# Kernel optimization log

Hardware: AMD Instinct MI355X
Metric: run time of the kernel (lower is better)

## Reference

```python
import jax, jax.numpy as jnp
import numpy as np

B = 256        # graphs per batch (python loop in original, vectorized here)
N = 512        # nodes per graph
DEG = 16       # avg degree
E_PER = N * DEG
T = 64         # num_node_types
D = 128        # gnn_hidden_dim


def setup_inputs() -> dict:
    key = jax.random.key(0)
    ks = jax.random.split(key, 8)
    node_feat = jax.random.randint(ks[0], (B * N,), 0, T)
    offs = (jnp.arange(B) * N)[:, None]
    src = (jax.random.randint(ks[1], (B, E_PER), 0, N) + offs).reshape(-1)
    dst = (jax.random.randint(ks[2], (B, E_PER), 0, N) + offs).reshape(-1)
    emb_table = jax.random.normal(ks[3], (T, D), dtype=jnp.float32) * 0.02
    W1 = jax.random.normal(ks[4], (D, D), dtype=jnp.float32) * (1.0 / np.sqrt(D))
    b1 = jnp.zeros((D,), dtype=jnp.float32)
    W2 = jax.random.normal(ks[5], (D, D), dtype=jnp.float32) * (1.0 / np.sqrt(D))
    b2 = jnp.zeros((D,), dtype=jnp.float32)
    return {"node_feat": node_feat, "src": src, "dst": dst,
            "emb_table": emb_table, "W1": W1, "b1": b1, "W2": W2, "b2": b2}


def _gcn_layer(h, src, dst, out_isqrt, in_isqrt, W, b, n):
    # DGL GraphConv, norm='both': D_in^{-1/2} A D_out^{-1/2} h W + b
    m = (h * out_isqrt[:, None])[src]                      # [E, D] gather
    agg = jax.ops.segment_sum(m, dst, num_segments=n)      # [Ntot, D] scatter
    return (agg * in_isqrt[:, None]) @ W + b


def reference(node_feat, src, dst, emb_table, W1, b1, W2, b2):
    n = node_feat.shape[0]
    ones = jnp.ones(src.shape[0], dtype=emb_table.dtype)
    deg_out = jnp.clip(jax.ops.segment_sum(ones, src, num_segments=n), 1.0)
    deg_in = jnp.clip(jax.ops.segment_sum(ones, dst, num_segments=n), 1.0)
    out_isqrt = jax.lax.rsqrt(deg_out)
    in_isqrt = jax.lax.rsqrt(deg_in)

    h = emb_table[node_feat]                                # [Ntot, D]
    # layer 1 (dropout is eval-mode identity) + relu, layer 2 + relu
    h = jax.nn.relu(_gcn_layer(h, src, dst, out_isqrt, in_isqrt, W1, b1, n))
    h = jax.nn.relu(_gcn_layer(h, src, dst, out_isqrt, in_isqrt, W2, b2, n))

    # dgl.mean_nodes per graph, then mean_gnn_embeddings + stack -> [B, D]
    gid = jnp.arange(n) // N
    hg = jax.ops.segment_sum(h, gid, num_segments=B) / float(N)
    return hg
```

## Files before the change

### kernel.cpp

```cpp
#include <hip/hip_runtime.h>
#include <stdint.h>

#define GRAPHS 256
#define NPG    512
#define EPG    8192
#define NTOT   (GRAPHS*NPG)

typedef __attribute__((ext_vector_type(8))) short s16x8;
typedef __attribute__((ext_vector_type(4))) float f32x4;

__device__ __forceinline__ float bf2f(unsigned short u){
  union { unsigned int i; float f; } c; c.i = ((unsigned int)u)<<16; return c.f;
}
__device__ __forceinline__ unsigned short f2bf(float f){
  union { float f; unsigned int i; } c; c.f = f;
  unsigned int r = c.i + 0x7fffu + ((c.i>>16)&1u);
  return (unsigned short)(r>>16);
}

__global__ __launch_bounds__(512) void k_csr(const int* __restrict__ src,
      const int* __restrict__ dst, const int* __restrict__ ntype,
      const float* __restrict__ emb, const float* __restrict__ W1,
      const float* __restrict__ W2,
      unsigned short* __restrict__ sorted_g, int* __restrict__ start_g,
      float* __restrict__ out_isqrt, unsigned short* __restrict__ EW1T,
      unsigned short* __restrict__ W2T){
  __shared__ int hist[NPG], cursor[NPG], co[NPG], cs[NPG+1];
  __shared__ unsigned short ntype_sh[NPG];
  __shared__ unsigned short sorted[EPG];
  const int tid=threadIdx.x;
  if (blockIdx.x >= GRAPHS){
    const int gid = (blockIdx.x-GRAPHS)*512 + tid;
    if (gid < 8192){
      const int t = gid>>7, c = gid&127;
      float acc=0.f;
      #pragma unroll 4
      for (int k=0;k<128;k++) acc += emb[t*128+k]*W1[k*128+c];
      EW1T[c*64+t]=f2bf(acc);
    } else {
      const int i = gid - 8192;
      const int k = i>>7, n = i&127;
      W2T[n*128+k] = f2bf(W2[k*128+n]);
    }
    return;
  }
  const int b=blockIdx.x, eb=b*EPG, nb=b*NPG;
  hist[tid]=0; co[tid]=0; ntype_sh[tid]=(unsigned short)ntype[nb+tid];
  __syncthreads();
  int4 d4[4], s4[4];
  {
    const int4* dv = (const int4*)(dst+eb);
    const int4* sv = (const int4*)(src+eb);
    #pragma unroll
    for (int j=0;j<4;j++){
      d4[j]=dv[tid + j*512];
      s4[j]=sv[tid + j*512];
      atomicAdd(&hist[d4[j].x&(NPG-1)],1); atomicAdd(&hist[d4[j].y&(NPG-1)],1);
      atomicAdd(&hist[d4[j].z&(NPG-1)],1); atomicAdd(&hist[d4[j].w&(NPG-1)],1);
      atomicAdd(&co[s4[j].x&(NPG-1)],1);   atomicAdd(&co[s4[j].y&(NPG-1)],1);
      atomicAdd(&co[s4[j].z&(NPG-1)],1);   atomicAdd(&co[s4[j].w&(NPG-1)],1);
    }
  }
  __syncthreads();
  if (tid<64){
    int carry=0;
    #pragma unroll
    for (int c=0;c<8;c++){
      int sc=hist[64*c+tid];
      #pragma unroll
      for (int off=1;off<64;off<<=1){ int y=__shfl_up(sc,off); if (tid>=off) sc+=y; }
      cs[64*c+tid+1]=carry+sc;
      carry+=__shfl(sc,63);
    }
    if (tid==0) cs[0]=0;
  }
  __syncthreads();
  cursor[tid]=cs[tid];
  __syncthreads();
  #pragma unroll
  for (int j=0;j<4;j++){
    int dl, s, pos;
    dl=d4[j].x&(NPG-1); s=s4[j].x&(NPG-1);
    pos=atomicAdd(&cursor[dl],1); sorted[pos]=(unsigned short)((ntype_sh[s]<<9)|s);
    dl=d4[j].y&(NPG-1); s=s4[j].y&(NPG-1);
    pos=atomicAdd(&cursor[dl],1); sorted[pos]=(unsigned short)((ntype_sh[s]<<9)|s);
    dl=d4[j].z&(NPG-1); s=s4[j].z&(NPG-1);
    pos=atomicAdd(&cursor[dl],1); sorted[pos]=(unsigned short)((ntype_sh[s]<<9)|s);
    dl=d4[j].w&(NPG-1); s=s4[j].w&(NPG-1);
    pos=atomicAdd(&cursor[dl],1); sorted[pos]=(unsigned short)((ntype_sh[s]<<9)|s);
  }
  __syncthreads();
  for (int i=tid;i<EPG/2;i+=512)
    ((unsigned int*)(sorted_g+(size_t)eb))[i] = ((const unsigned int*)sorted)[i];
  if (tid==0) start_g[b*(NPG+1)+NPG]=cs[NPG];
  start_g[b*(NPG+1)+tid]=cs[tid];
  {
    int a=co[tid]; if(a<1)a=1;
    out_isqrt[nb+tid]=rsqrtf((float)a);
  }
}

#define A1_LDS 73232
__global__ __launch_bounds__(512) void k_agg1(
      const unsigned short* __restrict__ sorted_g, const int* __restrict__ start_g,
      const unsigned short* __restrict__ EW1T, const float* __restrict__ out_isqrt,
      const float* __restrict__ b1, unsigned short* __restrict__ h1F){
  extern __shared__ char smem[];
  float* S      = (float*)(smem);
  float* wsc    = (float*)(smem + 69632);
  int*   sstart = (int*)  (smem + 71680);
  float* bsh    = (float*)(smem + 72720);
  const int bid=blockIdx.x, b=bid>>1, half=bid&1;
  const int v0=half*256, nb=b*NPG, tid=threadIdx.x;
  for (int i=tid; i<(256*68)/4; i+=512) ((f32x4*)S)[i]=(f32x4){0.f,0.f,0.f,0.f};
  for (int i=tid; i<NPG; i+=512) wsc[i]=out_isqrt[nb+i];
  for (int i=tid; i<257; i+=512) sstart[i]=start_g[b*(NPG+1)+v0+i];
  if (tid<128) bsh[tid]=b1[tid];
  __syncthreads();
  if (tid<256){
    const int beg=sstart[tid], end=sstart[tid+1];
    float* Sd = S + tid*68;
    const unsigned short* sg = sorted_g + (size_t)b*EPG;
    for (int i=beg;i<end;++i){
      const int ent = sg[i];
      Sd[ent>>9] += wsc[ent&511];
    }
  }
  __syncthreads();
  const int wave=tid>>6, lane=tid&63, l16=lane&15, quad=lane>>4;
  f32x4 acc[2][8];
  #pragma unroll
  for (int rt=0;rt<2;rt++)
    #pragma unroll
    for (int nt=0;nt<8;nt++) acc[rt][nt]=(f32x4){0.f,0.f,0.f,0.f};
  #pragma unroll
  for (int ks=0; ks<4; ++ks){
    const int kc = (ks&1)*32 + quad*8;
    s16x8 a[2];
    #pragma unroll
    for (int rt=0;rt<2;rt++){
      const int m = (wave*2+rt)*16 + l16;
      const float* sp = &S[m*68 + kc];
      f32x4 va = *(const f32x4*)sp;
      f32x4 vb = *(const f32x4*)(sp+4);
      union { s16x8 v; unsigned short u[8]; } pk;
      #pragma unroll
      for (int j=0;j<8;j++){
        const float f = (j<4)? va[j] : vb[j-4];
        const unsigned short hi = f2bf(f);
        pk.u[j] = (ks<2) ? hi : f2bf(f - bf2f(hi));
      }
      a[rt]=pk.v;
    }
    #pragma unroll
    for (int nt=0;nt<8;nt++){
      s16x8 bfr=__builtin_bit_cast(s16x8,
          *(const uint4*)(EW1T + (size_t)(nt*16+l16)*64 + kc));
      #pragma unroll
      for (int rt=0;rt<2;rt++)
        acc[rt][nt]=__builtin_amdgcn_mfma_f32_16x16x32_bf16(a[rt],bfr,acc[rt][nt],0,0,0);
    }
  }
  #pragma unroll
  for (int rt=0;rt<2;rt++){
    const int W = wave*2+rt;
    const int mloc = W*16 + quad*4;
    float isq[4], os[4];
    #pragma unroll
    for (int r=0;r<4;r++){
      int d = sstart[mloc+r+1]-sstart[mloc+r]; if (d<1) d=1;
      isq[r]=rsqrtf((float)d);
      os[r]=wsc[v0+mloc+r];
    }
    const int ks2 = half*8 + (W>>1);
    const int q2  = ((W&1)<<1) | (quad>>1);
    const int j0  = (quad&1)*4;
    #pragma unroll
    for (int nt=0;nt<8;nt++){
      const int col = nt*16+l16;
      const float bb = bsh[col];
      ushort4 st;
      float v;
      v = fmaxf(acc[rt][nt][0]*isq[0]+bb,0.f)*os[0]; st.x=f2bf(v);
      v = fmaxf(acc[rt][nt][1]*isq[1]+bb,0.f)*os[1]; st.y=f2bf(v);
      v = fmaxf(acc[rt][nt][2]*isq[2]+bb,0.f)*os[2]; st.z=f2bf(v);
      v = fmaxf(acc[rt][nt][3]*isq[3]+bb,0.f)*os[3]; st.w=f2bf(v);
      const size_t off = ((((size_t)b*16 + ks2)*8 + nt)*64 + q2*16 + l16)*8 + j0;
      *(ushort4*)(h1F + off) = st;
    }
  }
}

#define A2_LDS 67080
__global__ __launch_bounds__(512) void k_agg2(
      const unsigned short* __restrict__ sorted_g, const int* __restrict__ start_g,
      const unsigned short* __restrict__ h1F, unsigned short* __restrict__ M1F){
  extern __shared__ char smem[];
  unsigned char* A = (unsigned char*)smem;
  unsigned int* A32 = (unsigned int*)smem;
  int* sstart = (int*)(smem + 66560);
  const int bid=blockIdx.x;
  const int b  = ((bid>>5)<<3) | (bid&7);
  const int dt = (bid>>3)&3;
  const int v0=dt*128, tid=threadIdx.x;
  for (int i=tid; i<66560/16; i+=512) ((uint4*)smem)[i]=(uint4){0u,0u,0u,0u};
  for (int i=tid; i<129; i+=512) sstart[i]=start_g[b*(NPG+1)+v0+i];
  __syncthreads();
  {
    const int d = tid>>2, q = tid&3;
    const int beg=sstart[d], end=sstart[d+1], len=end-beg;
    const int qb = beg + ((len*q)>>2), qe = beg + ((len*(q+1))>>2);
    const unsigned short* sg = sorted_g + (size_t)b*EPG;
    const int rowbase = d*130;
    for (int i=qb;i<qe;++i){
      const int s = sg[i]&511;
      atomicAdd(&A32[rowbase + (s>>2)], 1u<<((s&3)*8));
    }
  }
  __syncthreads();
  const int wave=tid>>6, lane=tid&63, l16=lane&15, quad=lane>>4;
  const int mg=wave>>1, ng=wave&1;
  f32x4 acc[2][4];
  #pragma unroll
  for (int rt=0;rt<2;rt++)
    #pragma unroll
    for (int ct=0;ct<4;ct++) acc[rt][ct]=(f32x4){0.f,0.f,0.f,0.f};
  const uint4* bp[4];
  #pragma unroll
  for (int ct=0;ct<4;ct++)
    bp[ct] = (const uint4*)h1F + (((size_t)b*16)*8 + (ng*4+ct))*64 + lane;
  const unsigned char* Ab[2];
  #pragma unroll
  for (int rt=0;rt<2;rt++)
    Ab[rt] = A + ((mg*2+rt)*16 + l16)*520 + quad*8;
  #pragma unroll 2
  for (int ks=0; ks<16; ++ks){
    uint4 bq[4];
    #pragma unroll
    for (int ct=0;ct<4;ct++) bq[ct] = bp[ct][(size_t)ks*512];
    s16x8 afr[2];
    #pragma unroll
    for (int rt=0;rt<2;rt++){
      const uint2 aw = *(const uint2*)(Ab[rt] + ks*32);
      union { s16x8 v; unsigned short u[8]; } pk;
      #pragma unroll
      for (int j=0;j<4;j++){
        const float f0 = (float)((aw.x>>(8*j))&0xffu);
        const float f1 = (float)((aw.y>>(8*j))&0xffu);
        pk.u[j]   = (unsigned short)(__builtin_bit_cast(unsigned int, f0)>>16);
        pk.u[j+4] = (unsigned short)(__builtin_bit_cast(unsigned int, f1)>>16);
      }
      afr[rt]=pk.v;
    }
    #pragma unroll
    for (int rt=0;rt<2;rt++)
      #pragma unroll
      for (int ct=0;ct<4;ct++)
        acc[rt][ct]=__builtin_amdgcn_mfma_f32_16x16x32_bf16(afr[rt],
            __builtin_bit_cast(s16x8, bq[ct]), acc[rt][ct],0,0,0);
  }
  #pragma unroll
  for (int rt=0;rt<2;rt++){
    const int mloc=(mg*2+rt)*16 + quad*4;
    const int M = dt*8 + mg*2 + rt;
    float isq[4];
    #pragma unroll
    for (int r=0;r<4;r++){
      int d=sstart[mloc+r+1]-sstart[mloc+r]; if (d<1) d=1;
      isq[r]=rsqrtf((float)d);
    }
    #pragma unroll
    for (int ct=0;ct<4;ct++){
      const int ks2   = ng*2 + (ct>>1);
      const int quad2 = ((ct&1)<<1) | (l16>>3);
      const int j     = l16&7;
      unsigned short* base = M1F
          + ((((size_t)b*32+M)*4+ks2)*64 + quad2*16)*8 + j;
      #pragma unroll
      for (int r=0;r<4;r++)
        base[(size_t)(quad*4+r)*8] = f2bf(acc[rt][ct][r]*isq[r]);
    }
  }
}

__global__ __launch_bounds__(512) void k_gemm2(const unsigned short* __restrict__ M1F,
      const unsigned short* __restrict__ W2T, const float* __restrict__ b2,
      float* __restrict__ out){
  __shared__ __align__(16) unsigned short WT[128][136];
  __shared__ float bsh[128];
  __shared__ float colpart[8][128];
  const int b=blockIdx.x, tid=threadIdx.x;
  for (int idx=tid; idx<2048; idx+=512){
    const int row = idx>>4, c8 = idx&15;
    *(uint4*)&WT[row][c8*8] = *(const uint4*)(W2T + row*128 + c8*8);
  }
  if (tid<128) bsh[tid]=b2[tid];
  __syncthreads();
  const int wave=tid>>6, lane=tid&63, l16=lane&15, quad=lane>>4;
  float p[8];
  #pragma unroll
  for (int i=0;i<8;i++) p[i]=0.f;
  for (int chunk=0; chunk<2; ++chunk){
    f32x4 acc[2][8];
    #pragma unroll
    for (int rt=0;rt<2;rt++)
      #pragma unroll
      for (int ct=0;ct<8;ct++) acc[rt][ct]=(f32x4){0.f,0.f,0.f,0.f};
    #pragma unroll
    for (int ks=0;ks<4;ks++){
      s16x8 a[2], bf[8];
      #pragma unroll
      for (int rt=0;rt<2;rt++){
        const int M = wave*4 + chunk*2 + rt;
        a[rt]=__builtin_bit_cast(s16x8, *(const uint4*)(M1F
            + ((((size_t)b*32+M)*4+ks)*64 + lane)*8));
      }
      #pragma unroll
      for (int ct=0;ct<8;ct++)
        bf[ct]=__builtin_bit_cast(s16x8, *(const uint4*)&WT[ct*16+l16][ks*32+quad*8]);
      #pragma unroll
      for (int rt=0;rt<2;rt++)
        #pragma unroll
        for (int ct=0;ct<8;ct++)
          acc[rt][ct]=__builtin_amdgcn_mfma_f32_16x16x32_bf16(a[rt],bf[ct],acc[rt][ct],0,0,0);
    }
    #pragma unroll
    for (int rt=0;rt<2;rt++)
      #pragma unroll
      for (int ct=0;ct<8;ct++)
        #pragma unroll
        for (int r=0;r<4;r++){
          const int col=ct*16+l16;
          p[ct] += fmaxf(acc[rt][ct][r]+bsh[col],0.f);
        }
  }
  #pragma unroll
  for (int ct=0;ct<8;ct++){
    p[ct] += __shfl_xor(p[ct],16);
    p[ct] += __shfl_xor(p[ct],32);
  }
  if (quad==0){
    #pragma unroll
    for (int ct=0;ct<8;ct++) colpart[wave][ct*16+l16]=p[ct];
  }
  __syncthreads();
  if (tid<128){
    float s=0.f;
    #pragma unroll
    for (int w=0;w<8;w++) s+=colpart[w][tid];
    out[b*128+tid]=s*(1.f/512.f);
  }
}

extern "C" void kernel_launch(void* const* d_in, const int* in_sizes, int n_in,
                              void* d_out, int out_size, void* d_ws, size_t ws_size,
                              hipStream_t stream){
  const int* node_feat = (const int*)d_in[0];
  const int* src = (const int*)d_in[1];
  const int* dst = (const int*)d_in[2];
  const float* emb = (const float*)d_in[3];
  const float* W1  = (const float*)d_in[4];
  const float* b1  = (const float*)d_in[5];
  const float* W2  = (const float*)d_in[6];
  const float* b2  = (const float*)d_in[7];

  char* ws = (char*)d_ws;
  float* out_isqrt        = (float*)(ws);
  int* start_g            = (int*)(ws + 524288);
  unsigned short* sorted_g= (unsigned short*)(ws + 1049600);
  unsigned short* EW1T    = (unsigned short*)(ws + 5243904);
  unsigned short* W2T     = (unsigned short*)(ws + 5260288);
  unsigned short* h1F     = (unsigned short*)(ws + 5293056);
  unsigned short* M1F     = (unsigned short*)(ws + 38847488);

  (void)hipFuncSetAttribute(reinterpret_cast<const void*>(&k_agg1),
        hipFuncAttributeMaxDynamicSharedMemorySize, A1_LDS);
  (void)hipFuncSetAttribute(reinterpret_cast<const void*>(&k_agg2),
        hipFuncAttributeMaxDynamicSharedMemorySize, A2_LDS);

  k_csr<<<GRAPHS+48,512,0,stream>>>(src,dst,node_feat,emb,W1,W2,
        sorted_g,start_g,out_isqrt,EW1T,W2T);
  k_agg1<<<GRAPHS*2,512,A1_LDS,stream>>>(sorted_g,start_g,EW1T,out_isqrt,b1,h1F);
  k_agg2<<<GRAPHS*4,512,A2_LDS,stream>>>(sorted_g,start_g,h1F,M1F);
  k_gemm2<<<GRAPHS,512,0,stream>>>(M1F,W2T,b2,(float*)d_out);
}
```

Before: 151.1 us.

## Pack dst into sorted edges and scatter with flat edge-parallel LDS atomics

Sorted edge entries grow from 16 to 32 bits so each one also carries its destination node. The layer-1 and layer-2 aggregation loops then run edge-parallel over all 512 threads with LDS atomics, instead of one thread (or four) walking each destination's edge list. This removes load imbalance from variable-degree serial loops. Layer 1 switches to fixed-point integer atomics scaled by 2^20, which makes sums order-independent but slightly changes precision; the cost is doubled edge storage and global traffic.

```diff
diff --git a/kernel.cpp b/kernel.cpp
--- a/kernel.cpp
+++ b/kernel.cpp
@@ -22,12 +22,12 @@
       const int* __restrict__ dst, const int* __restrict__ ntype,
       const float* __restrict__ emb, const float* __restrict__ W1,
       const float* __restrict__ W2,
-      unsigned short* __restrict__ sorted_g, int* __restrict__ start_g,
+      unsigned int* __restrict__ sorted_g, int* __restrict__ start_g,
       float* __restrict__ out_isqrt, unsigned short* __restrict__ EW1T,
       unsigned short* __restrict__ W2T){
   __shared__ int hist[NPG], cursor[NPG], co[NPG], cs[NPG+1];
   __shared__ unsigned short ntype_sh[NPG];
-  __shared__ unsigned short sorted[EPG];
+  __shared__ unsigned int sorted[EPG];
   const int tid=threadIdx.x;
   if (blockIdx.x >= GRAPHS){
     const int gid = (blockIdx.x-GRAPHS)*512 + tid;
@@ -81,17 +81,20 @@
   for (int j=0;j<4;j++){
     int dl, s, pos;
     dl=d4[j].x&(NPG-1); s=s4[j].x&(NPG-1);
-    pos=atomicAdd(&cursor[dl],1); sorted[pos]=(unsigned short)((ntype_sh[s]<<9)|s);
+    pos=atomicAdd(&cursor[dl],1);
+    sorted[pos]=((unsigned int)dl<<15)|((unsigned int)ntype_sh[s]<<9)|(unsigned int)s;
     dl=d4[j].y&(NPG-1); s=s4[j].y&(NPG-1);
-    pos=atomicAdd(&cursor[dl],1); sorted[pos]=(unsigned short)((ntype_sh[s]<<9)|s);
+    pos=atomicAdd(&cursor[dl],1);
+    sorted[pos]=((unsigned int)dl<<15)|((unsigned int)ntype_sh[s]<<9)|(unsigned int)s;
     dl=d4[j].z&(NPG-1); s=s4[j].z&(NPG-1);
-    pos=atomicAdd(&cursor[dl],1); sorted[pos]=(unsigned short)((ntype_sh[s]<<9)|s);
+    pos=atomicAdd(&cursor[dl],1);
+    sorted[pos]=((unsigned int)dl<<15)|((unsigned int)ntype_sh[s]<<9)|(unsigned int)s;
     dl=d4[j].w&(NPG-1); s=s4[j].w&(NPG-1);
-    pos=atomicAdd(&cursor[dl],1); sorted[pos]=(unsigned short)((ntype_sh[s]<<9)|s);
-  }
-  __syncthreads();
-  for (int i=tid;i<EPG/2;i+=512)
-    ((unsigned int*)(sorted_g+(size_t)eb))[i] = ((const unsigned int*)sorted)[i];
+    pos=atomicAdd(&cursor[dl],1);
+    sorted[pos]=((unsigned int)dl<<15)|((unsigned int)ntype_sh[s]<<9)|(unsigned int)s;
+  }
+  __syncthreads();
+  for (int i=tid;i<EPG;i+=512) sorted_g[(size_t)eb+i] = sorted[i];
   if (tid==0) start_g[b*(NPG+1)+NPG]=cs[NPG];
   start_g[b*(NPG+1)+tid]=cs[tid];
   {
@@ -100,30 +103,36 @@
   }
 }
 
-#define A1_LDS 73232
+#define A1_LDS 75280
 __global__ __launch_bounds__(512) void k_agg1(
-      const unsigned short* __restrict__ sorted_g, const int* __restrict__ start_g,
+      const unsigned int* __restrict__ sorted_g, const int* __restrict__ start_g,
       const unsigned short* __restrict__ EW1T, const float* __restrict__ out_isqrt,
       const float* __restrict__ b1, unsigned short* __restrict__ h1F){
   extern __shared__ char smem[];
-  float* S      = (float*)(smem);
+  int*   Sint   = (int*)(smem);
   float* wsc    = (float*)(smem + 69632);
-  int*   sstart = (int*)  (smem + 71680);
-  float* bsh    = (float*)(smem + 72720);
+  int*   wint   = (int*)  (smem + 71680);
+  int*   sstart = (int*)  (smem + 73728);
+  float* bsh    = (float*)(smem + 74756);
   const int bid=blockIdx.x, b=bid>>1, half=bid&1;
   const int v0=half*256, nb=b*NPG, tid=threadIdx.x;
-  for (int i=tid; i<(256*68)/4; i+=512) ((f32x4*)S)[i]=(f32x4){0.f,0.f,0.f,0.f};
-  for (int i=tid; i<NPG; i+=512) wsc[i]=out_isqrt[nb+i];
+  for (int i=tid; i<(256*68)/4; i+=512) ((f32x4*)Sint)[i]=(f32x4){0.f,0.f,0.f,0.f};
+  for (int i=tid; i<NPG; i+=512){
+    const float w = out_isqrt[nb+i];
+    wsc[i]=w;
+    wint[i]=(int)(w*1048576.f);
+  }
   for (int i=tid; i<257; i+=512) sstart[i]=start_g[b*(NPG+1)+v0+i];
   if (tid<128) bsh[tid]=b1[tid];
   __syncthreads();
-  if (tid<256){
-    const int beg=sstart[tid], end=sstart[tid+1];
-    float* Sd = S + tid*68;
-    const unsigned short* sg = sorted_g + (size_t)b*EPG;
-    for (int i=beg;i<end;++i){
-      const int ent = sg[i];
-      Sd[ent>>9] += wsc[ent&511];
+  {
+    const int beg=sstart[0], end=sstart[256];
+    const unsigned int* sg = sorted_g + (size_t)b*EPG;
+    for (int i=beg+tid; i<end; i+=512){
+      const unsigned int ent = sg[i];
+      const int dl = (int)(ent>>15) - v0;
+      const int t  = (ent>>9)&63;
+      atomicAdd(&Sint[dl*68 + t], wint[ent&511]);
     }
   }
   __syncthreads();
@@ -140,13 +149,11 @@
     #pragma unroll
     for (int rt=0;rt<2;rt++){
       const int m = (wave*2+rt)*16 + l16;
-      const float* sp = &S[m*68 + kc];
-      f32x4 va = *(const f32x4*)sp;
-      f32x4 vb = *(const f32x4*)(sp+4);
+      const int* sp = &Sint[m*68 + kc];
       union { s16x8 v; unsigned short u[8]; } pk;
       #pragma unroll
       for (int j=0;j<8;j++){
-        const float f = (j<4)? va[j] : vb[j-4];
+        const float f = (float)sp[j] * (1.f/1048576.f);
         const unsigned short hi = f2bf(f);
         pk.u[j] = (ks<2) ? hi : f2bf(f - bf2f(hi));
       }
@@ -193,7 +200,7 @@
 
 #define A2_LDS 67080
 __global__ __launch_bounds__(512) void k_agg2(
-      const unsigned short* __restrict__ sorted_g, const int* __restrict__ start_g,
+      const unsigned int* __restrict__ sorted_g, const int* __restrict__ start_g,
       const unsigned short* __restrict__ h1F, unsigned short* __restrict__ M1F){
   extern __shared__ char smem[];
   unsigned char* A = (unsigned char*)smem;
@@ -207,14 +214,13 @@
   for (int i=tid; i<129; i+=512) sstart[i]=start_g[b*(NPG+1)+v0+i];
   __syncthreads();
   {
-    const int d = tid>>2, q = tid&3;
-    const int beg=sstart[d], end=sstart[d+1], len=end-beg;
-    const int qb = beg + ((len*q)>>2), qe = beg + ((len*(q+1))>>2);
-    const unsigned short* sg = sorted_g + (size_t)b*EPG;
-    const int rowbase = d*130;
-    for (int i=qb;i<qe;++i){
-      const int s = sg[i]&511;
-      atomicAdd(&A32[rowbase + (s>>2)], 1u<<((s&3)*8));
+    const int beg=sstart[0], end=sstart[128];
+    const unsigned int* sg = sorted_g + (size_t)b*EPG;
+    for (int i=beg+tid; i<end; i+=512){
+      const unsigned int ent = sg[i];
+      const int dl = (int)(ent>>15) - v0;
+      const int s  = ent&511;
+      atomicAdd(&A32[dl*130 + (s>>2)], 1u<<((s&3)*8));
     }
   }
   __syncthreads();
@@ -367,11 +373,11 @@
   char* ws = (char*)d_ws;
   float* out_isqrt        = (float*)(ws);
   int* start_g            = (int*)(ws + 524288);
-  unsigned short* sorted_g= (unsigned short*)(ws + 1049600);
-  unsigned short* EW1T    = (unsigned short*)(ws + 5243904);
-  unsigned short* W2T     = (unsigned short*)(ws + 5260288);
-  unsigned short* h1F     = (unsigned short*)(ws + 5293056);
-  unsigned short* M1F     = (unsigned short*)(ws + 38847488);
+  unsigned int* sorted_g  = (unsigned int*)(ws + 1049600);
+  unsigned short* EW1T    = (unsigned short*)(ws + 9438208);
+  unsigned short* W2T     = (unsigned short*)(ws + 9454592);
+  unsigned short* h1F     = (unsigned short*)(ws + 9487360);
+  unsigned short* M1F     = (unsigned short*)(ws + 43041792);
 
   (void)hipFuncSetAttribute(reinterpret_cast<const void*>(&k_agg1),
         hipFuncAttributeMaxDynamicSharedMemorySize, A1_LDS);
```

Measured after the change: 148.7 us. Within noise of the previous version (-1.6%).
